# Kernel tuning notes

Hardware: AMD Instinct MI355X
Metric: run time of the kernel (lower is better)

## Reference

```python
import jax, jax.numpy as jnp
import numpy as np

B, S, E, HEADS = 2, 2048, 2048, 16


def setup_inputs() -> dict:
    key = jax.random.key(0)
    k1, k2, k3 = jax.random.split(key, 3)
    x = jax.random.normal(k1, (B, S, E), dtype=jnp.float32)
    # Linear weights stored as (in, out); torch uses y = x @ W.T with W (out, in) -- same math.
    W_qkvh = jax.random.normal(k2, (E, 3 * E + HEADS), dtype=jnp.float32) * (E ** -0.5)
    W_out = jax.random.normal(k3, (E, E), dtype=jnp.float32) * (E ** -0.5)
    return {"x": x, "W_qkvh": W_qkvh, "W_out": W_out}


def reference(x, W_qkvh, W_out):
    b, s, e = x.shape
    heads = W_qkvh.shape[1] - 3 * e
    d = e // heads
    scale = e ** 0.5

    proj = x @ W_qkvh                                  # (b, s, 3e + heads)
    QKV, Hg = proj[..., : 3 * e], proj[..., 3 * e:]
    Hg = jnp.tanh(Hg).transpose(0, 2, 1)[..., None]    # (b, h, s, 1) gate
    QKV = QKV.reshape(b, s, heads, 3 * d).transpose(0, 2, 1, 3)  # (b, h, s, 3d)
    Q, K, V = jnp.split(QKV, 3, axis=-1)               # each (b, h, s, d)

    # Cummean(H*K) along seq: cumsum(n * x) / n^2 with n = 1..s
    n = jnp.arange(1, s + 1, dtype=x.dtype).reshape(1, 1, s, 1)
    Kc = jnp.cumsum(n * (Hg * K), axis=2) / (n * n)    # (b, h, s, d)

    scores = jnp.einsum('bhqd,bhkd->bhqk', Q, Kc) / scale
    causal = jnp.triu(jnp.ones((s, s), dtype=bool), k=1)
    scores = jnp.where(causal, -jnp.inf, scores)
    attn = jax.nn.softmax(scores, axis=-1)

    out = jnp.einsum('bhqk,bhkd->bhqd', attn, V)       # (b, h, s, d)
    out = out.transpose(0, 2, 1, 3).reshape(b, s, e)
    return out @ W_out
```

## Files before the change

kernel.cpp:

```cpp
#include <hip/hip_runtime.h>
#include <hip/hip_bf16.h>
#include <math.h>

#define PB 2
#define PS 2048
#define PE 2048
#define PH 16
#define PD 128
#define PN_PROJ 6160
#define PM 4096

typedef __attribute__((ext_vector_type(8))) short bf16x8;
typedef __attribute__((ext_vector_type(4))) float f32x4;

__device__ __forceinline__ void gload_lds16(const void* g, void* l) {
  __builtin_amdgcn_global_load_lds((const __attribute__((address_space(1))) void*)g,
                                   (__attribute__((address_space(3))) void*)l, 16, 0, 0);
}

__global__ __launch_bounds__(512, 1) void gemm_qkv(
    const __hip_bfloat16* __restrict__ A, const __hip_bfloat16* __restrict__ Bt,
    __hip_bfloat16* __restrict__ Qp, __hip_bfloat16* __restrict__ Kp,
    __hip_bfloat16* __restrict__ Vp, int K, int nTilesX) {
  constexpr int BM = 128, BN = 384, WM = 2, WN = 4;
  constexpr int MF = BM / WM / 16;
  constexpr int NF = BN / WN / 16;
  constexpr int SLOT = (BM + BN) * 64;
  constexpr int AL = BM / 64;
  constexpr int BL = BN / 64;
  constexpr int NLD = AL + BL;

  __shared__ __align__(16) __hip_bfloat16 lds[2 * SLOT];

  const int tid = threadIdx.x;
  const int w = tid >> 6, lane = tid & 63;
  const int fq = lane >> 4, fr = lane & 15;
  const int wm = w / WN, wn = w % WN;

  const int total = gridDim.x;
  const int swz = (blockIdx.x & 7) * (total >> 3) + (blockIdx.x >> 3);
  const int mBase = (swz / nTilesX) * BM;
  const int h = swz % nTilesX;
  const int nBase = h * BN;

  const int srow = tid >> 3, sc = tid & 7;

  auto stage = [&](int t) {
    char* base = (char*)lds + (size_t)(t & 1) * SLOT * 2;
#pragma unroll
    for (int l = 0; l < AL; ++l) {
      int row = l * 64 + srow;
      int cs = sc ^ (row & 7);
      gload_lds16(A + (size_t)(mBase + row) * K + t * 64 + cs * 8,
                  base + l * 8192 + w * 1024);
    }
#pragma unroll
    for (int l = 0; l < BL; ++l) {
      int row = l * 64 + srow;
      int cs = sc ^ (row & 7);
      gload_lds16(Bt + (size_t)(nBase + row) * K + t * 64 + cs * 8,
                  base + BM * 128 + l * 8192 + w * 1024);
    }
  };

  f32x4 acc[MF][NF];
#pragma unroll
  for (int m = 0; m < MF; ++m)
#pragma unroll
    for (int n = 0; n < NF; ++n) acc[m][n] = (f32x4){0.f, 0.f, 0.f, 0.f};

  const int NT = K / 64;
  stage(0); stage(1);

#pragma unroll 1
  for (int t = 0; t < NT; ++t) {
    if (t + 1 < NT) asm volatile("s_waitcnt vmcnt(%0)" ::"i"(NLD) : "memory");
    else            asm volatile("s_waitcnt vmcnt(0)" ::: "memory");
    __builtin_amdgcn_s_barrier();
    __builtin_amdgcn_sched_barrier(0);

    const __hip_bfloat16* sl = lds + (size_t)(t & 1) * SLOT;

    bf16x8 av[MF], bv[NF];
#pragma unroll
    for (int m = 0; m < MF; ++m) {
      int row = wm * (BM / WM) + m * 16 + fr;
      av[m] = *(const bf16x8*)&sl[row * 64 + ((fq ^ (row & 7)) * 8)];
    }
#pragma unroll
    for (int n = 0; n < NF; ++n) {
      int row = wn * (BN / WN) + n * 16 + fr;
      bv[n] = *(const bf16x8*)&sl[BM * 64 + row * 64 + ((fq ^ (row & 7)) * 8)];
    }
    asm volatile("s_waitcnt lgkmcnt(0)" ::: "memory");
    __builtin_amdgcn_sched_barrier(0);
    __builtin_amdgcn_s_setprio(1);
#pragma unroll
    for (int m = 0; m < MF; ++m)
#pragma unroll
      for (int n = 0; n < NF; ++n)
        acc[m][n] = __builtin_amdgcn_mfma_f32_16x16x32_bf16(av[m], bv[n], acc[m][n], 0, 0, 0);
    __builtin_amdgcn_s_setprio(0);

#pragma unroll
    for (int m = 0; m < MF; ++m) {
      int row = wm * (BM / WM) + m * 16 + fr;
      av[m] = *(const bf16x8*)&sl[row * 64 + (((4 + fq) ^ (row & 7)) * 8)];
    }
#pragma unroll
    for (int n = 0; n < NF; ++n) {
      int row = wn * (BN / WN) + n * 16 + fr;
      bv[n] = *(const bf16x8*)&sl[BM * 64 + row * 64 + (((4 + fq) ^ (row & 7)) * 8)];
    }
    asm volatile("s_waitcnt lgkmcnt(0)" ::: "memory");
    __builtin_amdgcn_s_barrier();
    __builtin_amdgcn_sched_barrier(0);
    if (t + 2 < NT) stage(t + 2);
    __builtin_amdgcn_s_setprio(1);
#pragma unroll
    for (int m = 0; m < MF; ++m)
#pragma unroll
      for (int n = 0; n < NF; ++n)
        acc[m][n] = __builtin_amdgcn_mfma_f32_16x16x32_bf16(av[m], bv[n], acc[m][n], 0, 0, 0);
    __builtin_amdgcn_s_setprio(0);
  }

#pragma unroll
  for (int m = 0; m < MF; ++m) {
#pragma unroll
    for (int n = 0; n < NF; ++n) {
      int row0 = mBase + wm * (BM / WM) + m * 16 + fq * 4;
      int colL = wn * (BN / WN) + n * 16 + fr;
      int which = colL >> 7;
      int d = colL & 127;
      __hip_bfloat16* dst = which == 0 ? Qp : (which == 1 ? Kp : Vp);
#pragma unroll
      for (int j = 0; j < 4; ++j) {
        int row = row0 + j;
        int b = row >> 11, s = row & (PS - 1);
        dst[(((size_t)(b * PH + h)) * PS + s) * PD + d] = __float2bfloat16(acc[m][n][j]);
      }
    }
  }
}

template <int BM, int BN, int WM, int WN, typename OutT>
__global__ __launch_bounds__(512, 1) void gemm_cs3(
    const __hip_bfloat16* __restrict__ A, const __hip_bfloat16* __restrict__ Bt,
    OutT* __restrict__ C, int K, int lda, int ldb, int ldc, int nTilesX) {
  constexpr int MF = BM / WM / 16;
  constexpr int NF = BN / WN / 16;
  constexpr int SLOT = (BM + BN) * 64;
  constexpr int AL = BM / 64;
  constexpr int BL = BN / 64;
  constexpr int NLD = AL + BL;

  __shared__ __align__(16) __hip_bfloat16 lds[3 * SLOT];

  const int tid = threadIdx.x;
  const int w = tid >> 6, lane = tid & 63;
  const int fq = lane >> 4, fr = lane & 15;
  const int wm = w / WN, wn = w % WN;

  const int total = gridDim.x;
  const int swz = (blockIdx.x & 7) * (total >> 3) + (blockIdx.x >> 3);
  const int mBase = (swz / nTilesX) * BM;
  const int nBase = (swz % nTilesX) * BN;

  const int srow = tid >> 3, sc = tid & 7;

  auto stage = [&](int t) {
    char* base = (char*)lds + (size_t)(t % 3) * SLOT * 2;
#pragma unroll
    for (int l = 0; l < AL; ++l) {
      int row = l * 64 + srow;
      int cs = sc ^ (row & 7);
      gload_lds16(A + (size_t)(mBase + row) * lda + t * 64 + cs * 8,
                  base + l * 8192 + w * 1024);
    }
#pragma unroll
    for (int l = 0; l < BL; ++l) {
      int row = l * 64 + srow;
      int cs = sc ^ (row & 7);
      gload_lds16(Bt + (size_t)(nBase + row) * ldb + t * 64 + cs * 8,
                  base + BM * 128 + l * 8192 + w * 1024);
    }
  };

  f32x4 acc[MF][NF];
#pragma unroll
  for (int m = 0; m < MF; ++m)
#pragma unroll
    for (int n = 0; n < NF; ++n) acc[m][n] = (f32x4){0.f, 0.f, 0.f, 0.f};

  const int NT = K / 64;
  stage(0); stage(1);

#pragma unroll 1
  for (int t = 0; t < NT; ++t) {
    if (t + 1 < NT) asm volatile("s_waitcnt vmcnt(%0)" ::"i"(NLD) : "memory");
    else            asm volatile("s_waitcnt vmcnt(0)" ::: "memory");
    __builtin_amdgcn_s_barrier();
    __builtin_amdgcn_sched_barrier(0);
    if (t + 2 < NT) stage(t + 2);

    const __hip_bfloat16* sl = lds + (size_t)(t % 3) * SLOT;

#pragma unroll
    for (int kk = 0; kk < 2; ++kk) {
      bf16x8 av[MF], bv[NF];
#pragma unroll
      for (int m = 0; m < MF; ++m) {
        int row = wm * (BM / WM) + m * 16 + fr;
        av[m] = *(const bf16x8*)&sl[row * 64 + (((kk * 4 + fq) ^ (row & 7)) * 8)];
      }
#pragma unroll
      for (int n = 0; n < NF; ++n) {
        int row = wn * (BN / WN) + n * 16 + fr;
        bv[n] = *(const bf16x8*)&sl[BM * 64 + row * 64 + (((kk * 4 + fq) ^ (row & 7)) * 8)];
      }
      asm volatile("s_waitcnt lgkmcnt(0)" ::: "memory");
      __builtin_amdgcn_sched_barrier(0);
      __builtin_amdgcn_s_setprio(1);
#pragma unroll
      for (int m = 0; m < MF; ++m)
#pragma unroll
        for (int n = 0; n < NF; ++n)
          acc[m][n] = __builtin_amdgcn_mfma_f32_16x16x32_bf16(av[m], bv[n], acc[m][n], 0, 0, 0);
      __builtin_amdgcn_s_setprio(0);
    }
  }

#pragma unroll
  for (int m = 0; m < MF; ++m) {
#pragma unroll
    for (int n = 0; n < NF; ++n) {
      int row0 = mBase + wm * (BM / WM) + m * 16 + fq * 4;
      int col = nBase + wn * (BN / WN) + n * 16 + fr;
#pragma unroll
      for (int j = 0; j < 4; ++j) {
        if constexpr (__is_same(OutT, float))
          C[(size_t)(row0 + j) * ldc + col] = acc[m][n][j];
        else
          C[(size_t)(row0 + j) * ldc + col] = __float2bfloat16(acc[m][n][j]);
      }
    }
  }
}

__global__ __launch_bounds__(256) void transpose_cast(const float* __restrict__ W,
                                                      __hip_bfloat16* __restrict__ Wt,
                                                      int ldw, int ldt, int nOff) {
  __shared__ float t[32][33];
  int nb = blockIdx.x * 32, kb = blockIdx.y * 32;
  int tx = threadIdx.x & 31, ty = threadIdx.x >> 5;
#pragma unroll
  for (int i = 0; i < 4; ++i) {
    int k = ty + i * 8;
    t[k][tx] = W[(size_t)(kb + k) * ldw + nOff + nb + tx];
  }
  __syncthreads();
#pragma unroll
  for (int i = 0; i < 4; ++i) {
    int n = ty + i * 8;
    Wt[(size_t)(nb + n) * ldt + kb + tx] = __float2bfloat16(t[tx][n]);
  }
}

__global__ __launch_bounds__(256) void hg_from_x(const float* __restrict__ x,
                                                 const float* __restrict__ W,
                                                 float* __restrict__ hgbuf,
                                                 __hip_bfloat16* __restrict__ xb) {
  int bs = blockIdx.x;
  int b = bs >> 11, s = bs & (PS - 1);
  __shared__ float xs[PE];
  __shared__ float red[16][17];
  const float* xr = x + (size_t)bs * PE;
  for (int i = threadIdx.x; i < PE / 4; i += 256)
    *(float4*)&xs[i * 4] = ((const float4*)xr)[i];
  __syncthreads();
  {
    union { __hip_bfloat16 hh[8]; bf16x8 v; } pk;
#pragma unroll
    for (int k = 0; k < 8; ++k) pk.hh[k] = __float2bfloat16(xs[threadIdx.x * 8 + k]);
    *(bf16x8*)&xb[(size_t)bs * PE + threadIdx.x * 8] = pk.v;
  }
  int h = threadIdx.x & 15, part = threadIdx.x >> 4;
  float acc = 0.f;
  for (int k = part * 128; k < part * 128 + 128; ++k)
    acc += xs[k] * W[(size_t)k * PN_PROJ + 3 * PE + h];
  red[part][h] = acc;
  __syncthreads();
  if (threadIdx.x < 16) {
    float sm = 0.f;
#pragma unroll
    for (int p = 0; p < 16; ++p) sm += red[p][threadIdx.x];
    hgbuf[(size_t)(b * PH + threadIdx.x) * PS + s] = tanhf(sm);
  }
}

#define KC_SCALE 0.022097086912079608f

__global__ __launch_bounds__(128) void kc_pass1(const __hip_bfloat16* __restrict__ Kp,
                                                const float* __restrict__ hgbuf,
                                                float* __restrict__ csum) {
  int c = blockIdx.x & 15, bh = blockIdx.x >> 4;
  int d = threadIdx.x;
  __shared__ float hgs[128];
  hgs[d] = hgbuf[(size_t)bh * PS + c * 128 + d];
  __syncthreads();
  const __hip_bfloat16* kb = Kp + ((size_t)bh * PS + c * 128) * PD + d;
  float acc = 0.f;
  int j0 = c * 128;
  for (int i = 0; i < 128; ++i)
    acc += (float)(j0 + i + 1) * hgs[i] * __bfloat162float(kb[(size_t)i * PD]);
  csum[blockIdx.x * 128 + d] = acc;
}

__global__ __launch_bounds__(128) void kc_pass2(__hip_bfloat16* __restrict__ Kp,
                                                const float* __restrict__ hgbuf,
                                                const float* __restrict__ csum) {
  int c = blockIdx.x & 15, bh = blockIdx.x >> 4;
  int d = threadIdx.x;
  __shared__ float hgs[128];
  hgs[d] = hgbuf[(size_t)bh * PS + c * 128 + d];
  __syncthreads();
  float acc = 0.f;
  for (int cc = 0; cc < c; ++cc) acc += csum[(bh * 16 + cc) * 128 + d];
  __hip_bfloat16* kb = Kp + ((size_t)bh * PS + c * 128) * PD + d;
  int j0 = c * 128;
  for (int i = 0; i < 128; ++i) {
    float t = (float)(j0 + i + 1);
    acc += t * hgs[i] * __bfloat162float(kb[(size_t)i * PD]);
    kb[(size_t)i * PD] = __float2bfloat16(acc / (t * t) * KC_SCALE);
  }
}

__global__ __launch_bounds__(256) void vt_pack(const __hip_bfloat16* __restrict__ Vp,
                                               __hip_bfloat16* __restrict__ Vtp) {
  int sc = blockIdx.x & 31, bh = blockIdx.x >> 5;
  int s0 = sc * 64;
  int tid = threadIdx.x;
  __shared__ __align__(16) __hip_bfloat16 Vlds[64][136];
  const __hip_bfloat16* src = Vp + ((size_t)bh * PS + s0) * PD;
#pragma unroll
  for (int it = 0; it < 4; ++it) {
    int i = it * 256 + tid;
    int row = i >> 4, ch = i & 15;
    *(bf16x8*)&Vlds[row][ch * 8] = *(const bf16x8*)&src[(size_t)row * PD + ch * 8];
  }
  __syncthreads();
  int d = tid >> 1, half = tid & 1;
  __hip_bfloat16* dst = Vtp + ((size_t)bh * PD + d) * PS + s0 + half * 32;
#pragma unroll
  for (int c8 = 0; c8 < 8; ++c8) {
    union { __hip_bfloat16 h4[4]; uint2 u; } pk;
#pragma unroll
    for (int k = 0; k < 4; ++k) pk.h4[k] = Vlds[half * 32 + c8 * 4 + k][d];
    *(uint2*)&dst[c8 * 4] = pk.u;
  }
}

__global__ __launch_bounds__(256) void attn_mfma(const __hip_bfloat16* __restrict__ Qp,
                                                 const __hip_bfloat16* __restrict__ Kp,
                                                 const __hip_bfloat16* __restrict__ Vtp,
                                                 __hip_bfloat16* __restrict__ O) {
  const int bid = (blockIdx.x & 7) * 32 + (blockIdx.x >> 3);
  const int bh = bid >> 3, pk = bid & 7;
  const int b = bh >> 4, h = bh & 15;
  const int tid = threadIdx.x;
  const int w = tid >> 6, lane = tid & 63;
  const int fq = lane >> 4, fr = lane & 15;

  __shared__ __align__(16) char smem[120832];
  __hip_bfloat16* Psw = (__hip_bfloat16*)(smem + 65536) + w * 32 * 72;
  __hip_bfloat16* Os = (__hip_bfloat16*)(smem + 84480);

  const __hip_bfloat16* kb0 = Kp + (size_t)bh * PS * PD;
  const __hip_bfloat16* vb0 = Vtp + (size_t)bh * PD * PS;

  const int klr = lane >> 4, kc = lane & 15;
  const int vlr = lane >> 3, vc = lane & 7;

  auto stageKV = [&](int t, int bufi) {
    char* ksb = smem + bufi * 16384;
    char* vsb = smem + 32768 + bufi * 16384;
    const __hip_bfloat16* kb = kb0 + (size_t)(t * 64) * PD;
    const __hip_bfloat16* vb = vb0 + t * 64;
#pragma unroll
    for (int p = 0; p < 4; ++p) {
      int row = w * 16 + p * 4 + klr;
      int cs = kc ^ (row & 7);
      gload_lds16(kb + (size_t)row * PD + cs * 8, ksb + (w * 16 + p * 4) * 256);
    }
#pragma unroll
    for (int p = 0; p < 4; ++p) {
      int row = w * 32 + p * 8 + vlr;
      int cs = vc ^ (row & 7);
      gload_lds16(vb + (size_t)row * PS + cs * 8, vsb + (w * 32 + p * 8) * 128);
    }
  };

  stageKV(0, 0);
  int cur = 0;

#pragma unroll 1
  for (int phase = 0; phase < 2; ++phase) {
    const int qt = (phase == 0) ? pk : 15 - pk;
    const int nt = (qt + 1) * 2;
    const int q0 = qt * 128;
    const int qw = q0 + w * 32;

    const __hip_bfloat16* qbase = Qp + ((size_t)bh * PS + qw) * PD;
    bf16x8 qf[2][4];
#pragma unroll
    for (int r2 = 0; r2 < 2; ++r2)
#pragma unroll
      for (int kk = 0; kk < 4; ++kk)
        qf[r2][kk] = *(const bf16x8*)&qbase[(size_t)(r2 * 16 + fr) * PD + kk * 32 + fq * 8];

    f32x4 oacc[2][8];
#pragma unroll
    for (int r2 = 0; r2 < 2; ++r2)
#pragma unroll
      for (int nd = 0; nd < 8; ++nd) oacc[r2][nd] = (f32x4){0.f, 0.f, 0.f, 0.f};
    float m_[2] = {-__builtin_inff(), -__builtin_inff()};
    float l_[2] = {0.f, 0.f};

#pragma unroll 1
    for (int kt = 0; kt < nt; ++kt) {
      const bool hasNext = (kt + 1 < nt) || (phase == 0);
      if (hasNext) stageKV((kt + 1 < nt) ? kt + 1 : 0, cur ^ 1);

      if (kt * 64 <= qw + 31) {
        const __hip_bfloat16* Ks = (const __hip_bfloat16*)(smem + cur * 16384);
        const __hip_bfloat16* Vts = (const __hip_bfloat16*)(smem + 32768 + cur * 16384);
        const bool diag = (kt * 64 + 63) > qw;

        f32x4 sacc[2][4];
#pragma unroll
        for (int r2 = 0; r2 < 2; ++r2)
#pragma unroll
          for (int n = 0; n < 4; ++n) sacc[r2][n] = (f32x4){0.f, 0.f, 0.f, 0.f};
#pragma unroll
        for (int kk = 0; kk < 4; ++kk) {
#pragma unroll
          for (int n = 0; n < 4; ++n) {
            bf16x8 kf = *(const bf16x8*)&Ks[(n * 16 + fr) * 128 + (((kk * 4 + fq) ^ (fr & 7)) * 8)];
            sacc[0][n] = __builtin_amdgcn_mfma_f32_16x16x32_bf16(kf, qf[0][kk], sacc[0][n], 0, 0, 0);
            sacc[1][n] = __builtin_amdgcn_mfma_f32_16x16x32_bf16(kf, qf[1][kk], sacc[1][n], 0, 0, 0);
          }
        }

#pragma unroll
        for (int r2 = 0; r2 < 2; ++r2) {
          const int qg = qw + r2 * 16 + fr;
          float sv[4][4];
#pragma unroll
          for (int n = 0; n < 4; ++n)
#pragma unroll
            for (int j = 0; j < 4; ++j) {
              float s = sacc[r2][n][j];
              if (diag && (kt * 64 + n * 16 + fq * 4 + j) > qg) s = -__builtin_inff();
              sv[n][j] = s;
            }
          float pmax = sv[0][0];
#pragma unroll
          for (int n = 0; n < 4; ++n)
#pragma unroll
            for (int j = 0; j < 4; ++j) pmax = fmaxf(pmax, sv[n][j]);
          pmax = fmaxf(pmax, __shfl_xor(pmax, 16, 64));
          pmax = fmaxf(pmax, __shfl_xor(pmax, 32, 64));

          const bool nof = __all(pmax <= m_[r2] + 8.f);
          const float mn = nof ? m_[r2] : fmaxf(m_[r2], pmax);
          float ps = 0.f;
#pragma unroll
          for (int n = 0; n < 4; ++n) {
            union { __hip_bfloat16 hh[4]; uint2 u; } pkk;
#pragma unroll
            for (int j = 0; j < 4; ++j) {
              float p = __expf(sv[n][j] - mn);
              ps += p;
              pkk.hh[j] = __float2bfloat16(p);
            }
            *(uint2*)&Psw[(r2 * 16 + fr) * 72 + n * 16 + fq * 4] = pkk.u;
          }
          ps += __shfl_xor(ps, 16, 64);
          ps += __shfl_xor(ps, 32, 64);

          if (!nof) {
            const float alpha = __expf(m_[r2] - mn);
            l_[r2] = l_[r2] * alpha + ps;
            m_[r2] = mn;
            float a0 = __shfl(alpha, fq * 4 + 0, 64);
            float a1 = __shfl(alpha, fq * 4 + 1, 64);
            float a2 = __shfl(alpha, fq * 4 + 2, 64);
            float a3 = __shfl(alpha, fq * 4 + 3, 64);
#pragma unroll
            for (int nd = 0; nd < 8; ++nd) {
              oacc[r2][nd][0] *= a0; oacc[r2][nd][1] *= a1;
              oacc[r2][nd][2] *= a2; oacc[r2][nd][3] *= a3;
            }
          } else {
            l_[r2] += ps;
          }
        }

#pragma unroll
        for (int kk2 = 0; kk2 < 2; ++kk2) {
          bf16x8 pa0 = *(const bf16x8*)&Psw[(0 * 16 + fr) * 72 + kk2 * 32 + fq * 8];
          bf16x8 pa1 = *(const bf16x8*)&Psw[(1 * 16 + fr) * 72 + kk2 * 32 + fq * 8];
#pragma unroll
          for (int nd = 0; nd < 8; ++nd) {
            bf16x8 vf = *(const bf16x8*)&Vts[(nd * 16 + fr) * 64 + (((kk2 * 4 + fq) ^ (fr & 7)) * 8)];
            oacc[0][nd] = __builtin_amdgcn_mfma_f32_16x16x32_bf16(pa0, vf, oacc[0][nd], 0, 0, 0);
            oacc[1][nd] = __builtin_amdgcn_mfma_f32_16x16x32_bf16(pa1, vf, oacc[1][nd], 0, 0, 0);
          }
        }
      }

      __syncthreads();
      cur ^= 1;
    }

    float i0 = 1.0f / l_[0], i1 = 1.0f / l_[1];
    float inv4[2][4];
#pragma unroll
    for (int j = 0; j < 4; ++j) {
      inv4[0][j] = __shfl(i0, fq * 4 + j, 64);
      inv4[1][j] = __shfl(i1, fq * 4 + j, 64);
    }
#pragma unroll
    for (int r2 = 0; r2 < 2; ++r2)
#pragma unroll
      for (int nd = 0; nd < 8; ++nd)
#pragma unroll
        for (int j = 0; j < 4; ++j)
          Os[(w * 32 + r2 * 16 + fq * 4 + j) * 136 + nd * 16 + fr] =
              __float2bfloat16(oacc[r2][nd][j] * inv4[r2][j]);
    __syncthreads();
#pragma unroll
    for (int it = 0; it < 8; ++it) {
      int i = it * 256 + tid;
      int row = i >> 4, ch = i & 15;
      *(bf16x8*)&O[(size_t)(b * PS + q0 + row) * PE + h * 128 + ch * 8] =
          *(const bf16x8*)&Os[row * 136 + ch * 8];
    }
  }
}

extern "C" void kernel_launch(void* const* d_in, const int* in_sizes, int n_in,
                              void* d_out, int out_size, void* d_ws, size_t ws_size,
                              hipStream_t stream) {
  const float* x     = (const float*)d_in[0];
  const float* Wqkvh = (const float*)d_in[1];
  const float* Wout  = (const float*)d_in[2];
  float* out = (float*)d_out;

  const size_t HD = (size_t)PB * PH * PS * PD;
  char* wsb = (char*)d_ws;
  __hip_bfloat16* Qp = (__hip_bfloat16*)wsb;   wsb += HD * 2;
  __hip_bfloat16* Kp = (__hip_bfloat16*)wsb;   wsb += HD * 2;
  __hip_bfloat16* Vp = (__hip_bfloat16*)wsb;   wsb += HD * 2;
  __hip_bfloat16* Vtp = (__hip_bfloat16*)wsb;  wsb += HD * 2;
  __hip_bfloat16* xb = (__hip_bfloat16*)wsb;   wsb += (size_t)PM * PE * 2;
  __hip_bfloat16* Wq_t = (__hip_bfloat16*)wsb; wsb += (size_t)3 * PE * PE * 2;
  __hip_bfloat16* Wout_t = (__hip_bfloat16*)wsb; wsb += (size_t)PE * PE * 2;
  float* hgbuf = (float*)wsb;                  wsb += (size_t)PB * PH * PS * 4;
  float* csum = (float*)wsb;

  hg_from_x<<<PM, 256, 0, stream>>>(x, Wqkvh, hgbuf, xb);
  transpose_cast<<<dim3(3 * PE / 32, PE / 32), 256, 0, stream>>>(Wqkvh, Wq_t, PN_PROJ, PE, 0);
  transpose_cast<<<dim3(PE / 32, PE / 32), 256, 0, stream>>>(Wout, Wout_t, PE, PE, 0);

  gemm_qkv<<<dim3((PM / 128) * PH), 512, 0, stream>>>(xb, Wq_t, Qp, Kp, Vp, PE, PH);

  kc_pass1<<<PB * PH * 16, 128, 0, stream>>>(Kp, hgbuf, csum);
  kc_pass2<<<PB * PH * 16, 128, 0, stream>>>(Kp, hgbuf, csum);

  vt_pack<<<PB * PH * 32, 256, 0, stream>>>(Vp, Vtp);
  __hip_bfloat16* Ob = xb;
  attn_mfma<<<PB * PH * 8, 256, 0, stream>>>(Qp, Kp, Vtp, Ob);

  gemm_cs3<128, 256, 2, 4, float>
      <<<dim3((PM / 128) * (PE / 256)), 512, 0, stream>>>(
          Ob, Wout_t, out, PE, PE, PE, PE, PE / 256);
}
```

Before: 313.2 us.

## Write V transposed from QKV GEMM epilogue and fold log2e into score scale

```diff
diff --git a/kernel.cpp b/kernel.cpp
--- a/kernel.cpp
+++ b/kernel.cpp
@@ -21,7 +21,7 @@
 __global__ __launch_bounds__(512, 1) void gemm_qkv(
     const __hip_bfloat16* __restrict__ A, const __hip_bfloat16* __restrict__ Bt,
     __hip_bfloat16* __restrict__ Qp, __hip_bfloat16* __restrict__ Kp,
-    __hip_bfloat16* __restrict__ Vp, int K, int nTilesX) {
+    __hip_bfloat16* __restrict__ Vtp, int K, int nTilesX) {
   constexpr int BM = 128, BN = 384, WM = 2, WN = 4;
   constexpr int MF = BM / WM / 16;
   constexpr int NF = BN / WN / 16;
@@ -133,12 +133,17 @@
       int colL = wn * (BN / WN) + n * 16 + fr;
       int which = colL >> 7;
       int d = colL & 127;
-      __hip_bfloat16* dst = which == 0 ? Qp : (which == 1 ? Kp : Vp);
-#pragma unroll
-      for (int j = 0; j < 4; ++j) {
-        int row = row0 + j;
-        int b = row >> 11, s = row & (PS - 1);
-        dst[(((size_t)(b * PH + h)) * PS + s) * PD + d] = __float2bfloat16(acc[m][n][j]);
+      int b = row0 >> 11, s0 = row0 & (PS - 1);
+      if (which == 2) {
+        union { __hip_bfloat16 hh[4]; uint2 u; } pk;
+#pragma unroll
+        for (int j = 0; j < 4; ++j) pk.hh[j] = __float2bfloat16(acc[m][n][j]);
+        *(uint2*)&Vtp[(((size_t)(b * PH + h)) * PD + d) * PS + s0] = pk.u;
+      } else {
+        __hip_bfloat16* dst = which == 0 ? Qp : Kp;
+#pragma unroll
+        for (int j = 0; j < 4; ++j)
+          dst[(((size_t)(b * PH + h)) * PS + s0 + j) * PD + d] = __float2bfloat16(acc[m][n][j]);
       }
     }
   }
@@ -299,7 +304,7 @@
   }
 }
 
-#define KC_SCALE 0.022097086912079608f
+#define KC_SCALE 0.031879358f
 
 __global__ __launch_bounds__(128) void kc_pass1(const __hip_bfloat16* __restrict__ Kp,
                                                 const float* __restrict__ hgbuf,
@@ -336,31 +341,6 @@
   }
 }
 
-__global__ __launch_bounds__(256) void vt_pack(const __hip_bfloat16* __restrict__ Vp,
-                                               __hip_bfloat16* __restrict__ Vtp) {
-  int sc = blockIdx.x & 31, bh = blockIdx.x >> 5;
-  int s0 = sc * 64;
-  int tid = threadIdx.x;
-  __shared__ __align__(16) __hip_bfloat16 Vlds[64][136];
-  const __hip_bfloat16* src = Vp + ((size_t)bh * PS + s0) * PD;
-#pragma unroll
-  for (int it = 0; it < 4; ++it) {
-    int i = it * 256 + tid;
-    int row = i >> 4, ch = i & 15;
-    *(bf16x8*)&Vlds[row][ch * 8] = *(const bf16x8*)&src[(size_t)row * PD + ch * 8];
-  }
-  __syncthreads();
-  int d = tid >> 1, half = tid & 1;
-  __hip_bfloat16* dst = Vtp + ((size_t)bh * PD + d) * PS + s0 + half * 32;
-#pragma unroll
-  for (int c8 = 0; c8 < 8; ++c8) {
-    union { __hip_bfloat16 h4[4]; uint2 u; } pk;
-#pragma unroll
-    for (int k = 0; k < 4; ++k) pk.h4[k] = Vlds[half * 32 + c8 * 4 + k][d];
-    *(uint2*)&dst[c8 * 4] = pk.u;
-  }
-}
-
 __global__ __launch_bounds__(256) void attn_mfma(const __hip_bfloat16* __restrict__ Qp,
                                                  const __hip_bfloat16* __restrict__ Kp,
                                                  const __hip_bfloat16* __restrict__ Vtp,
@@ -472,7 +452,7 @@
           pmax = fmaxf(pmax, __shfl_xor(pmax, 16, 64));
           pmax = fmaxf(pmax, __shfl_xor(pmax, 32, 64));
 
-          const bool nof = __all(pmax <= m_[r2] + 8.f);
+          const bool nof = __all(pmax <= m_[r2] + 11.5415605f);
           const float mn = nof ? m_[r2] : fmaxf(m_[r2], pmax);
           float ps = 0.f;
 #pragma unroll
@@ -480,7 +460,7 @@
             union { __hip_bfloat16 hh[4]; uint2 u; } pkk;
 #pragma unroll
             for (int j = 0; j < 4; ++j) {
-              float p = __expf(sv[n][j] - mn);
+              float p = exp2f(sv[n][j] - mn);
               ps += p;
               pkk.hh[j] = __float2bfloat16(p);
             }
@@ -490,7 +470,7 @@
           ps += __shfl_xor(ps, 32, 64);
 
           if (!nof) {
-            const float alpha = __expf(m_[r2] - mn);
+            const float alpha = exp2f(m_[r2] - mn);
             l_[r2] = l_[r2] * alpha + ps;
             m_[r2] = mn;
             float a0 = __shfl(alpha, fq * 4 + 0, 64);
@@ -562,7 +542,6 @@
   char* wsb = (char*)d_ws;
   __hip_bfloat16* Qp = (__hip_bfloat16*)wsb;   wsb += HD * 2;
   __hip_bfloat16* Kp = (__hip_bfloat16*)wsb;   wsb += HD * 2;
-  __hip_bfloat16* Vp = (__hip_bfloat16*)wsb;   wsb += HD * 2;
   __hip_bfloat16* Vtp = (__hip_bfloat16*)wsb;  wsb += HD * 2;
   __hip_bfloat16* xb = (__hip_bfloat16*)wsb;   wsb += (size_t)PM * PE * 2;
   __hip_bfloat16* Wq_t = (__hip_bfloat16*)wsb; wsb += (size_t)3 * PE * PE * 2;
@@ -574,12 +553,11 @@
   transpose_cast<<<dim3(3 * PE / 32, PE / 32), 256, 0, stream>>>(Wqkvh, Wq_t, PN_PROJ, PE, 0);
   transpose_cast<<<dim3(PE / 32, PE / 32), 256, 0, stream>>>(Wout, Wout_t, PE, PE, 0);
 
-  gemm_qkv<<<dim3((PM / 128) * PH), 512, 0, stream>>>(xb, Wq_t, Qp, Kp, Vp, PE, PH);
+  gemm_qkv<<<dim3((PM / 128) * PH), 512, 0, stream>>>(xb, Wq_t, Qp, Kp, Vtp, PE, PH);
 
   kc_pass1<<<PB * PH * 16, 128, 0, stream>>>(Kp, hgbuf, csum);
   kc_pass2<<<PB * PH * 16, 128, 0, stream>>>(Kp, hgbuf, csum);
 
-  vt_pack<<<PB * PH * 32, 256, 0, stream>>>(Vp, Vtp);
   __hip_bfloat16* Ob = xb;
   attn_mfma<<<PB * PH * 8, 256, 0, stream>>>(Qp, Kp, Vtp, Ob);
 
```

Result: no change. 313.9 us (+0.2%).
